# Performance work log

Measured on AMD Instinct MI355X. Metric: run time of the kernel, lower is better.

## Reference

```python
import jax, jax.numpy as jnp
import numpy as np

B, S, H, NH, HD, F, L = 512, 32, 1024, 16, 64, 2048, 6
OBS_D, REF_D, ACT_D, MAX_REL = 256, 128, 32, 32
SCALE = 1.0 / np.sqrt(HD)
LN_EPS = 1e-5


def _ln(x, g, b):
    mu = x.mean(-1, keepdims=True)
    var = ((x - mu) ** 2).mean(-1, keepdims=True)
    return (x - mu) * jax.lax.rsqrt(var + LN_EPS) * g + b


def _mlp3(x, w0, b0, w1, b1, w2, b2):
    h = jax.nn.relu(x @ w0 + b0)
    h = jax.nn.relu(h @ w1 + b1)
    return h @ w2 + b2


def setup_inputs() -> dict:
    key = jax.random.key(0)
    ks = iter(jax.random.split(key, 64))

    def n(shape, scale=1.0):
        return (jax.random.normal(next(ks), shape, dtype=jnp.float32) * scale)

    W = 0.02  # weight scale (xavier-ish) to keep activations sane
    inp = {
        'obs': n((B, S, OBS_D)), 'ref': n((B, S, REF_D)),
        'obs_w0': n((OBS_D, 512), W), 'obs_b0': jnp.zeros((512,), jnp.float32),
        'obs_w1': n((512, 256), W), 'obs_b1': jnp.zeros((256,), jnp.float32),
        'obs_w2': n((256, H), W), 'obs_b2': jnp.zeros((H,), jnp.float32),
        'ref_w0': n((REF_D, 256), W), 'ref_b0': jnp.zeros((256,), jnp.float32),
        'ref_w1': n((256, 256), W), 'ref_b1': jnp.zeros((256,), jnp.float32),
        'ref_w2': n((256, H), W), 'ref_b2': jnp.zeros((H,), jnp.float32),
        'pos_emb': n((64, H), W),
        'Wq': n((L, H, H), W), 'Wk': n((L, H, H), W), 'Wv': n((L, H, H), W),
        'Wo': n((L, H, H), W), 'bo': jnp.zeros((L, H), jnp.float32),
        'rel_emb': n((L, 2 * MAX_REL + 1, HD), W),
        'ff_w1': n((L, H, F), W), 'ff_b1': jnp.zeros((L, F), jnp.float32),
        'ff_w2': n((L, F, H), W), 'ff_b2': jnp.zeros((L, H), jnp.float32),
        'ln1_g': jnp.ones((L, H), jnp.float32), 'ln1_b': jnp.zeros((L, H), jnp.float32),
        'ln2_g': jnp.ones((L, H), jnp.float32), 'ln2_b': jnp.zeros((L, H), jnp.float32),
        'act_w0': n((H, 256), W), 'act_b0': jnp.zeros((256,), jnp.float32),
        'act_w1': n((256, 128), W), 'act_b1': jnp.zeros((128,), jnp.float32),
        'act_w2': n((128, ACT_D), W), 'act_b2': jnp.zeros((ACT_D,), jnp.float32),
    }
    return inp


def _forward(obs, ref, obs_w0, obs_b0, obs_w1, obs_b1, obs_w2, obs_b2,
             ref_w0, ref_b0, ref_w1, ref_b1, ref_w2, ref_b2, pos_emb,
             Wq, Wk, Wv, Wo, bo, rel_emb, ff_w1, ff_b1, ff_w2, ff_b2,
             ln1_g, ln1_b, ln2_g, ln2_b,
             act_w0, act_b0, act_w1, act_b1, act_w2, act_b2):
    b, s, _ = obs.shape
    x = _mlp3(obs, obs_w0, obs_b0, obs_w1, obs_b1, obs_w2, obs_b2)
    x = x + _mlp3(ref, ref_w0, ref_b0, ref_w1, ref_b1, ref_w2, ref_b2)
    x = x + pos_emb[:s][None]  # learned positional encoding

    idx = jnp.arange(s)
    rel_idx = jnp.clip(idx[:, None] - idx[None, :], -MAX_REL, MAX_REL) + MAX_REL  # [S,S]

    def block(h, p):
        wq, wk, wv, wo, b_o, rel, w1, b1, w2, b2, g1, be1, g2, be2 = p
        xn = _ln(h, g1, be1)
        q = (xn @ wq).reshape(b, s, NH, HD)
        k = (xn @ wk).reshape(b, s, NH, HD)
        v = (xn @ wv).reshape(b, s, NH, HD)
        scores = jnp.einsum('bqhd,bkhd->bhqk', q, k) * SCALE
        rel_e = rel[rel_idx]  # [S,S,HD]
        scores = scores + jnp.einsum('bqhd,qkd->bhqk', q, rel_e)
        attn = jax.nn.softmax(scores, axis=-1)
        o = jnp.einsum('bhqk,bkhd->bqhd', attn, v).reshape(b, s, H)
        h = h + o @ wo + b_o
        xn2 = _ln(h, g2, be2)
        ff = jax.nn.gelu(xn2 @ w1 + b1, approximate=False) @ w2 + b2
        return h + ff, None

    x, _ = jax.lax.scan(block, x, (Wq, Wk, Wv, Wo, bo, rel_emb,
                                    ff_w1, ff_b1, ff_w2, ff_b2,
                                    ln1_g, ln1_b, ln2_g, ln2_b))
    return _mlp3(x[:, -1], act_w0, act_b0, act_w1, act_b1, act_w2, act_b2)


def reference(obs, ref, obs_w0, obs_b0, obs_w1, obs_b1, obs_w2, obs_b2,
              ref_w0, ref_b0, ref_w1, ref_b1, ref_w2, ref_b2, pos_emb,
              Wq, Wk, Wv, Wo, bo, rel_emb, ff_w1, ff_b1, ff_w2, ff_b2,
              ln1_g, ln1_b, ln2_g, ln2_b,
              act_w0, act_b0, act_w1, act_b1, act_w2, act_b2):
    return _forward(obs, ref, obs_w0, obs_b0, obs_w1, obs_b1, obs_w2, obs_b2,
                    ref_w0, ref_b0, ref_w1, ref_b1, ref_w2, ref_b2, pos_emb,
                    Wq, Wk, Wv, Wo, bo, rel_emb, ff_w1, ff_b1, ff_w2, ff_b2,
                    ln1_g, ln1_b, ln2_g, ln2_b,
                    act_w0, act_b0, act_w1, act_b1, act_w2, act_b2)
```

## Files before the change

### kernel.cpp

```cpp
#include <hip/hip_runtime.h>
#include <cstdint>
#include <cstddef>

typedef unsigned short u16;
typedef float f32x4 __attribute__((ext_vector_type(4)));
typedef short s16x8 __attribute__((ext_vector_type(8)));
typedef __bf16 bf16x8 __attribute__((ext_vector_type(8)));

#define DEVINL __device__ __forceinline__

DEVINL float bf2f(u16 u){ union{unsigned int i; float f;} c; c.i=((unsigned int)u)<<16; return c.f; }
DEVINL u16 f2bf(float f){ union{float f; unsigned int i;} c; c.f=f; unsigned int u=c.i;
                          u += 0x7FFF + ((u>>16)&1); return (u16)(u>>16); }

DEVINL f32x4 mfma16(bf16x8 a, bf16x8 b, f32x4 c){
  return __builtin_amdgcn_mfma_f32_16x16x32_bf16(a, b, c, 0, 0, 0);
}

typedef const __attribute__((address_space(1))) void* gas1p;
typedef __attribute__((address_space(3))) void* as3p;
DEVINL void async16(const void* g, void* l){
  __builtin_amdgcn_global_load_lds((gas1p)g, (as3p)l, 16, 0, 0);
}


__global__ void cvt_bf16(const float* __restrict__ in, u16* __restrict__ out, int n){
  int i = (blockIdx.x * 256 + threadIdx.x) * 4;
  if (i >= n) return;
  float4 v = *(const float4*)(in + i);
  short4 sv = make_short4((short)f2bf(v.x), (short)f2bf(v.y), (short)f2bf(v.z), (short)f2bf(v.w));
  *(short4*)(out + i) = sv;
}

__global__ __launch_bounds__(256) void trans_w(const float* __restrict__ W, u16* __restrict__ WT,
                                               int K, int N){
  __shared__ float t[32][33];
  const float* Wm = W  + (size_t)blockIdx.z * K * N;
  u16*         Tm = WT + (size_t)blockIdx.z * K * N;
  const int x = threadIdx.x, y = threadIdx.y;
  const int n0 = blockIdx.x * 32, k0 = blockIdx.y * 32;
#pragma unroll
  for (int j = 0; j < 32; j += 8)
    t[y + j][x] = Wm[(size_t)(k0 + y + j) * N + n0 + x];
  __syncthreads();
#pragma unroll
  for (int j = 0; j < 32; j += 8)
    Tm[(size_t)(n0 + y + j) * K + k0 + x] = f2bf(t[x][y + j]);
}


__global__ __launch_bounds__(256) void gemm128(
    const u16* __restrict__ A, const u16* __restrict__ BT,
    const float* __restrict__ bias, const float* __restrict__ resid,
    const float* __restrict__ pos, void* __restrict__ out,
    int M, int N, int K, int fuse)
{
  __shared__ u16 As[2][4096];
  __shared__ u16 Bs[2][4096];
  const int tid = threadIdx.x;

  const int nbn = gridDim.x;
  const int nwg = gridDim.x * gridDim.y;
  const int lid = blockIdx.y * nbn + blockIdx.x;
  const int q8 = nwg >> 3, r8 = nwg & 7;
  const int xcd = lid & 7, posi = lid >> 3;
  const int swz = (xcd < r8 ? xcd * (q8 + 1) : r8 * (q8 + 1) + (xcd - r8) * q8) + posi;
  const int bm = swz / nbn, bn = swz - bm * nbn;

  const int lane = tid & 63, wid = tid >> 6;
  const int lr = lane & 15, lk = lane >> 4;
  const int wm = (wid >> 1) * 64, wn = (wid & 1) * 64;

  f32x4 acc[4][4] = {};

  const int r0 = tid >> 2;
  const int c0 = (tid & 3) * 8;
  const u16* Ab = A  + (size_t)(bm * 128 + r0) * K + c0;
  const u16* Bb = BT + (size_t)(bn * 128 + r0) * K + c0;
  const size_t rstep = (size_t)64 * K;
  const int nk = K >> 5;

  async16(Ab,         &As[0][tid * 8]);
  async16(Ab + rstep, &As[0][2048 + tid * 8]);
  async16(Bb,         &Bs[0][tid * 8]);
  async16(Bb + rstep, &Bs[0][2048 + tid * 8]);

  int cur = 0;
  for (int kt = 0; kt < nk; ++kt){
    __syncthreads();
    if (kt + 1 < nk){
      const u16* An = Ab + (size_t)(kt + 1) * 32;
      const u16* Bn = Bb + (size_t)(kt + 1) * 32;
      u16* Asn = &As[cur ^ 1][0];
      u16* Bsn = &Bs[cur ^ 1][0];
      async16(An,         Asn + tid * 8);
      async16(An + rstep, Asn + 2048 + tid * 8);
      async16(Bn,         Bsn + tid * 8);
      async16(Bn + rstep, Bsn + 2048 + tid * 8);
    }
    bf16x8 af[4], bfv[4];
#pragma unroll
    for (int i = 0; i < 4; ++i)
      af[i] = *(const bf16x8*)&As[cur][(wm + i * 16 + lr) * 32 + lk * 8];
#pragma unroll
    for (int j = 0; j < 4; ++j)
      bfv[j] = *(const bf16x8*)&Bs[cur][(wn + j * 16 + lr) * 32 + lk * 8];
#pragma unroll
    for (int i = 0; i < 4; ++i)
#pragma unroll
      for (int j = 0; j < 4; ++j)
        acc[i][j] = mfma16(af[i], bfv[j], acc[i][j]);
    cur ^= 1;
  }

  const int gm0 = bm * 128 + wm, gn0 = bn * 128 + wn;
  float* outf = (float*)out;
  u16*   outb = (u16*)out;
#pragma unroll
  for (int i = 0; i < 4; ++i){
#pragma unroll
    for (int j = 0; j < 4; ++j){
      const int col = gn0 + j * 16 + lr;
      const float bv = bias ? bias[col] : 0.f;
#pragma unroll
      for (int r = 0; r < 4; ++r){
        const int row = gm0 + i * 16 + lk * 4 + r;
        const size_t idx = (size_t)row * N + col;
        float v = acc[i][j][r] + bv;
        if (fuse == 1)      v = fmaxf(v, 0.f);
        else if (fuse == 2) v = 0.5f * v * (1.f + erff(v * 0.70710678118654752f));
        else if (fuse == 4) v += resid[idx];
        else if (fuse == 5) v += resid[idx] + pos[((row & 31) << 10) + col];
        if (fuse >= 3) outf[idx] = v;
        else           outb[idx] = f2bf(v);
      }
    }
  }
}


__global__ __launch_bounds__(256) void ln_k(
    const float* __restrict__ x, const float* __restrict__ g,
    const float* __restrict__ b, u16* __restrict__ out)
{
  const int row = blockIdx.x;
  const float* xr = x + (size_t)row * 1024;
  const int tid = threadIdx.x;
  float4 v = *(const float4*)(xr + tid * 4);
  float s  = v.x + v.y + v.z + v.w;
  float ss = v.x * v.x + v.y * v.y + v.z * v.z + v.w * v.w;
#pragma unroll
  for (int m = 1; m < 64; m <<= 1){ s += __shfl_xor(s, m, 64); ss += __shfl_xor(ss, m, 64); }
  __shared__ float red[8];
  if ((tid & 63) == 0){ red[tid >> 6] = s; red[4 + (tid >> 6)] = ss; }
  __syncthreads();
  s  = red[0] + red[1] + red[2] + red[3];
  ss = red[4] + red[5] + red[6] + red[7];
  const float mu = s * (1.f / 1024.f);
  const float rs = rsqrtf(ss * (1.f / 1024.f) - mu * mu + 1e-5f);
  float4 gg = *(const float4*)(g + tid * 4);
  float4 bb = *(const float4*)(b + tid * 4);
  short4 sv = make_short4((short)f2bf((v.x - mu) * rs * gg.x + bb.x),
                          (short)f2bf((v.y - mu) * rs * gg.y + bb.y),
                          (short)f2bf((v.z - mu) * rs * gg.z + bb.z),
                          (short)f2bf((v.w - mu) * rs * gg.w + bb.w));
  *(short4*)(out + (size_t)row * 1024 + tid * 4) = sv;
}


__global__ __launch_bounds__(256) void attn_k(
    const u16* __restrict__ QKV, const u16* __restrict__ rel,
    u16* __restrict__ O)
{
  __shared__ char smem[65536];
  const int tid = threadIdx.x;
  const int wid = tid >> 6, lane = tid & 63;
  const int lr = lane & 15, lk = lane >> 4;
  char* sw = smem + wid * 16384;
  float* P = (float*)sw;
  u16*  AL = (u16*)(sw + 8704);
  u16*  VT = (u16*)(sw + 11264);

  const int pair = blockIdx.x * 4 + wid;
  const int b = pair >> 4, h = pair & 15;
  const u16* q  = QKV + (size_t)b * 32 * 3072 + (size_t)h * 64;
  const u16* kk = q + 1024;
  const u16* v  = q + 2048;
  u16* o = O + (size_t)b * 32768 + (size_t)h * 64;

  s16x8 vv[4];
#pragma unroll
  for (int j = 0; j < 4; ++j){
    const int e = j * 64 + lane;
    const int ki = e >> 3, d0 = (e & 7) * 8;
    vv[j] = *(const s16x8*)(v + (size_t)ki * 3072 + d0);
  }

  bf16x8 qf[2][2], kf[2][2];
#pragma unroll
  for (int mf = 0; mf < 2; ++mf)
#pragma unroll
    for (int ks = 0; ks < 2; ++ks){
      qf[mf][ks] = *(const bf16x8*)(q  + (size_t)(mf * 16 + lr) * 3072 + ks * 32 + lk * 8);
      kf[mf][ks] = *(const bf16x8*)(kk + (size_t)(mf * 16 + lr) * 3072 + ks * 32 + lk * 8);
    }

  f32x4 sc[2][2] = {};
#pragma unroll
  for (int mf = 0; mf < 2; ++mf)
#pragma unroll
    for (int nf = 0; nf < 2; ++nf){
      sc[mf][nf] = mfma16(qf[mf][0], kf[nf][0], sc[mf][nf]);
      sc[mf][nf] = mfma16(qf[mf][1], kf[nf][1], sc[mf][nf]);
      sc[mf][nf] *= 0.125f;
    }

  f32x4 p[2][4] = {};
#pragma unroll
  for (int nf = 0; nf < 4; ++nf){
    bf16x8 rf0 = *(const bf16x8*)(rel + (nf * 16 + lr) * 64 + lk * 8);
    bf16x8 rf1 = *(const bf16x8*)(rel + (nf * 16 + lr) * 64 + 32 + lk * 8);
#pragma unroll
    for (int mf = 0; mf < 2; ++mf){
      p[mf][nf] = mfma16(qf[mf][0], rf0, p[mf][nf]);
      p[mf][nf] = mfma16(qf[mf][1], rf1, p[mf][nf]);
    }
  }

#pragma unroll
  for (int j = 0; j < 4; ++j){
    const int e = j * 64 + lane;
    const int ki = e >> 3, d0 = (e & 7) * 8;
#pragma unroll
    for (int i = 0; i < 8; ++i)
      VT[(d0 + i) * 40 + ki] = (u16)vv[j][i];
  }
#pragma unroll
  for (int mf = 0; mf < 2; ++mf)
#pragma unroll
    for (int nf = 0; nf < 4; ++nf)
#pragma unroll
      for (int r = 0; r < 4; ++r)
        P[(mf * 16 + lk * 4 + r) * 68 + nf * 16 + lr] = p[mf][nf][r];

  __syncthreads();

#pragma unroll
  for (int mf = 0; mf < 2; ++mf)
#pragma unroll
    for (int n2 = 0; n2 < 2; ++n2)
#pragma unroll
      for (int r = 0; r < 4; ++r){
        const int qr = mf * 16 + lk * 4 + r;
        const int kc = n2 * 16 + lr;
        sc[mf][n2][r] += P[qr * 68 + (qr - kc + 32)];
      }

#pragma unroll
  for (int mf = 0; mf < 2; ++mf)
#pragma unroll
    for (int r = 0; r < 4; ++r){
      float mx = fmaxf(sc[mf][0][r], sc[mf][1][r]);
#pragma unroll
      for (int m2 = 1; m2 < 16; m2 <<= 1) mx = fmaxf(mx, __shfl_xor(mx, m2, 64));
      const float e0 = __expf(sc[mf][0][r] - mx);
      const float e1 = __expf(sc[mf][1][r] - mx);
      float sm = e0 + e1;
#pragma unroll
      for (int m2 = 1; m2 < 16; m2 <<= 1) sm += __shfl_xor(sm, m2, 64);
      const float inv = 1.f / sm;
      sc[mf][0][r] = e0 * inv;
      sc[mf][1][r] = e1 * inv;
    }

#pragma unroll
  for (int mf = 0; mf < 2; ++mf)
#pragma unroll
    for (int n2 = 0; n2 < 2; ++n2)
#pragma unroll
      for (int r = 0; r < 4; ++r)
        AL[(mf * 16 + lk * 4 + r) * 40 + n2 * 16 + lr] = f2bf(sc[mf][n2][r]);

  __syncthreads();

  bf16x8 paf[2];
  paf[0] = *(const bf16x8*)&AL[(lr) * 40 + lk * 8];
  paf[1] = *(const bf16x8*)&AL[(16 + lr) * 40 + lk * 8];

  f32x4 of[2][4] = {};
#pragma unroll
  for (int nf = 0; nf < 4; ++nf){
    bf16x8 vf = *(const bf16x8*)&VT[(nf * 16 + lr) * 40 + lk * 8];
    of[0][nf] = mfma16(paf[0], vf, of[0][nf]);
    of[1][nf] = mfma16(paf[1], vf, of[1][nf]);
  }
#pragma unroll
  for (int mf = 0; mf < 2; ++mf)
#pragma unroll
    for (int nf = 0; nf < 4; ++nf)
#pragma unroll
      for (int r = 0; r < 4; ++r)
        o[(size_t)(mf * 16 + lk * 4 + r) * 1024 + nf * 16 + lr] = f2bf(of[mf][nf][r]);
}


__global__ void gather_last(const float* __restrict__ x, u16* __restrict__ out){
  const int i = blockIdx.x * 256 + threadIdx.x;
  const int b = i >> 10, c = i & 1023;
  out[i] = f2bf(x[((size_t)b * 32 + 31) * 1024 + c]);
}

__global__ void small_gemm(const u16* __restrict__ A, const u16* __restrict__ BT,
                           const float* __restrict__ bias, void* __restrict__ out,
                           int M, int N, int K, int fuse){
  const int idx = blockIdx.x * 256 + threadIdx.x;
  if (idx >= M * N) return;
  const int m = idx / N, n = idx - m * N;
  const u16* a  = A  + (size_t)m * K;
  const u16* bt = BT + (size_t)n * K;
  float acc = 0.f;
  for (int k = 0; k < K; k += 8){
    s16x8 av = *(const s16x8*)(a + k);
    s16x8 bv = *(const s16x8*)(bt + k);
#pragma unroll
    for (int i = 0; i < 8; ++i) acc += bf2f((u16)av[i]) * bf2f((u16)bv[i]);
  }
  float v = acc + bias[n];
  if (fuse == 1) v = fmaxf(v, 0.f);
  if (fuse == 3) ((float*)out)[idx] = v;
  else           ((u16*)out)[idx]   = f2bf(v);
}


extern "C" void kernel_launch(void* const* d_in, const int* in_sizes, int n_in,
                              void* d_out, int out_size, void* d_ws, size_t ws_size,
                              hipStream_t stream)
{
  (void)in_sizes; (void)n_in; (void)out_size;
  const float* obs    = (const float*)d_in[0];
  const float* refp   = (const float*)d_in[1];
  const float* obs_w0 = (const float*)d_in[2];
  const float* obs_b0 = (const float*)d_in[3];
  const float* obs_w1 = (const float*)d_in[4];
  const float* obs_b1 = (const float*)d_in[5];
  const float* obs_w2 = (const float*)d_in[6];
  const float* obs_b2 = (const float*)d_in[7];
  const float* ref_w0 = (const float*)d_in[8];
  const float* ref_b0 = (const float*)d_in[9];
  const float* ref_w1 = (const float*)d_in[10];
  const float* ref_b1 = (const float*)d_in[11];
  const float* ref_w2 = (const float*)d_in[12];
  const float* ref_b2 = (const float*)d_in[13];
  const float* pos    = (const float*)d_in[14];
  const float* Wq     = (const float*)d_in[15];
  const float* Wk     = (const float*)d_in[16];
  const float* Wv     = (const float*)d_in[17];
  const float* Wo     = (const float*)d_in[18];
  const float* bo     = (const float*)d_in[19];
  const float* rel    = (const float*)d_in[20];
  const float* ff_w1  = (const float*)d_in[21];
  const float* ff_b1  = (const float*)d_in[22];
  const float* ff_w2  = (const float*)d_in[23];
  const float* ff_b2  = (const float*)d_in[24];
  const float* ln1g   = (const float*)d_in[25];
  const float* ln1b   = (const float*)d_in[26];
  const float* ln2g   = (const float*)d_in[27];
  const float* ln2b   = (const float*)d_in[28];
  const float* act_w0 = (const float*)d_in[29];
  const float* act_b0 = (const float*)d_in[30];
  const float* act_w1 = (const float*)d_in[31];
  const float* act_b1 = (const float*)d_in[32];
  const float* act_w2 = (const float*)d_in[33];
  const float* act_b2 = (const float*)d_in[34];
  float* outp = (float*)d_out;

  char* wsp = (char*)d_ws; size_t off = 0;
  auto alloc = [&](size_t bytes)->char*{ char* p = wsp + off;
                                         off = (off + bytes + 255) & ~(size_t)255; return p; };

  u16* wt_obs0 = (u16*)alloc((size_t)512 * 256 * 2);
  u16* wt_obs1 = (u16*)alloc((size_t)256 * 512 * 2);
  u16* wt_obs2 = (u16*)alloc((size_t)1024 * 256 * 2);
  u16* wt_ref0 = (u16*)alloc((size_t)256 * 128 * 2);
  u16* wt_ref1 = (u16*)alloc((size_t)256 * 256 * 2);
  u16* wt_ref2 = (u16*)alloc((size_t)1024 * 256 * 2);
  u16* wt_a0   = (u16*)alloc((size_t)256 * 1024 * 2);
  u16* wt_a1   = (u16*)alloc((size_t)128 * 256 * 2);
  u16* wt_a2   = (u16*)alloc((size_t)32 * 128 * 2);
  u16* rel_bf  = (u16*)alloc((size_t)6 * 65 * 64 * 2);
  u16* wt_qkv  = (u16*)alloc((size_t)3072 * 1024 * 2);
  u16* wt_lo   = (u16*)alloc((size_t)1024 * 1024 * 2);
  u16* wt_lf1  = (u16*)alloc((size_t)2048 * 1024 * 2);
  u16* wt_lf2  = (u16*)alloc((size_t)2048 * 1024 * 2);
  float* x     = (float*)alloc((size_t)16384 * 1024 * 4);
  u16* xn      = (u16*)alloc((size_t)16384 * 1024 * 2);
  u16* qkv     = (u16*)alloc((size_t)16384 * 3072 * 2);

  if (off > ws_size) return;

  u16* obs_bf = qkv;
  u16* h1     = qkv + (size_t)16384 * 256;
  u16* h2     = qkv + (size_t)16384 * 768;
  u16* ref_bf = xn;
  u16* ob     = xn;
  u16* ffb    = qkv;
  u16* xlast  = qkv;
  u16* a1b    = qkv + (size_t)16384 * 256;
  u16* a2b    = qkv + (size_t)16384 * 512;

  auto CV = [&](const float* src, u16* dst, int n){
    cvt_bf16<<<dim3((n / 4 + 255) / 256), dim3(256), 0, stream>>>(src, dst, n);
  };
  auto TR = [&](const float* W, u16* WT, int Kd, int Nd, int nz){
    trans_w<<<dim3(Nd / 32, Kd / 32, nz), dim3(32, 8), 0, stream>>>(W, WT, Kd, Nd);
  };
  auto GM = [&](const u16* A, const u16* BT, const float* bias, const float* resid,
                const float* posb, void* op, int Md, int Nd, int Kd, int fuse){
    gemm128<<<dim3(Nd / 128, Md / 128), dim3(256), 0, stream>>>(A, BT, bias, resid, posb, op, Md, Nd, Kd, fuse);
  };

  CV(rel, rel_bf, 6 * 65 * 64);
  TR(obs_w0, wt_obs0, 256, 512, 1);
  TR(obs_w1, wt_obs1, 512, 256, 1);
  TR(obs_w2, wt_obs2, 256, 1024, 1);
  TR(ref_w0, wt_ref0, 128, 256, 1);
  TR(ref_w1, wt_ref1, 256, 256, 1);
  TR(ref_w2, wt_ref2, 256, 1024, 1);
  TR(act_w0, wt_a0, 1024, 256, 1);
  TR(act_w1, wt_a1, 256, 128, 1);
  TR(act_w2, wt_a2, 128, 32, 1);

  const int M = 16384;
  CV(obs, obs_bf, 16384 * 256);
  GM(obs_bf, wt_obs0, obs_b0, nullptr, nullptr, h1, M, 512, 256, 1);
  GM(h1,     wt_obs1, obs_b1, nullptr, nullptr, h2, M, 256, 512, 1);
  GM(h2,     wt_obs2, obs_b2, nullptr, nullptr, x,  M, 1024, 256, 3);
  CV(refp, ref_bf, 16384 * 128);
  GM(ref_bf, wt_ref0, ref_b0, nullptr, nullptr, h2, M, 256, 128, 1);
  GM(h2,     wt_ref1, ref_b1, nullptr, nullptr, h1, M, 256, 256, 1);
  GM(h1,     wt_ref2, ref_b2, x, pos,           x,  M, 1024, 256, 5);

  for (int l = 0; l < 6; ++l){
    TR(Wq + (size_t)l * 1048576, wt_qkv,                        1024, 1024, 1);
    TR(Wk + (size_t)l * 1048576, wt_qkv + (size_t)1024 * 1024,  1024, 1024, 1);
    TR(Wv + (size_t)l * 1048576, wt_qkv + (size_t)2048 * 1024,  1024, 1024, 1);
    TR(Wo + (size_t)l * 1048576, wt_lo, 1024, 1024, 1);
    TR(ff_w1 + (size_t)l * 2097152, wt_lf1, 1024, 2048, 1);
    TR(ff_w2 + (size_t)l * 2097152, wt_lf2, 2048, 1024, 1);

    ln_k<<<dim3(16384), dim3(256), 0, stream>>>(x, ln1g + l * 1024, ln1b + l * 1024, xn);
    GM(xn, wt_qkv, nullptr, nullptr, nullptr, qkv, M, 3072, 1024, 0);
    attn_k<<<dim3(2048), dim3(256), 0, stream>>>(qkv, rel_bf + (size_t)l * 4160, ob);
    GM(ob, wt_lo, bo + l * 1024, x, nullptr, x, M, 1024, 1024, 4);
    ln_k<<<dim3(16384), dim3(256), 0, stream>>>(x, ln2g + l * 1024, ln2b + l * 1024, xn);
    GM(xn,  wt_lf1, ff_b1 + l * 2048, nullptr, nullptr, ffb, M, 2048, 1024, 2);
    GM(ffb, wt_lf2, ff_b2 + l * 1024, x, nullptr, x, M, 1024, 2048, 4);
  }

  gather_last<<<dim3(2048), dim3(256), 0, stream>>>(x, xlast);
  small_gemm<<<dim3(512 * 256 / 256), dim3(256), 0, stream>>>(xlast, wt_a0, act_b0, a1b, 512, 256, 1024, 1);
  small_gemm<<<dim3(512 * 128 / 256), dim3(256), 0, stream>>>(a1b, wt_a1, act_b1, a2b, 512, 128, 256, 1);
  small_gemm<<<dim3(512 * 32 / 256),  dim3(256), 0, stream>>>(a2b, wt_a2, act_b2, outp, 512, 32, 128, 3);
}
```

Measured before the change: 3.981 ms.

## Add 256x256-tile 8-wave GEMM with swizzled LDS and XCD-aware block remap

Adds a gemm256 kernel with 512 threads and 256x256 output tiles. It uses a double-buffered LDS staged via global_load_lds with an XOR swizzle, a four-phase MFMA schedule interleaved with prefetch, setprio hints, and a workgroup remap that groups tiles per XCD. It replaces gemm128 for all large-N GEMMs (QKV, Wo, FFN, and the obs/ref final layers). The larger tiles are meant to raise arithmetic intensity and cut global/L2 traffic, at the cost of higher register and LDS pressure, fewer workgroups per GEMM, and many barriers.

```diff
diff --git a/kernel.cpp b/kernel.cpp
--- a/kernel.cpp
+++ b/kernel.cpp
@@ -22,6 +22,8 @@
 DEVINL void async16(const void* g, void* l){
   __builtin_amdgcn_global_load_lds((gas1p)g, (as3p)l, 16, 0, 0);
 }
+
+#define SWZ(b) ((b) ^ ((((b) >> 9) & 1) << 5))
 
 
 __global__ void cvt_bf16(const float* __restrict__ in, u16* __restrict__ out, int n){
@@ -127,6 +129,173 @@
         const int row = gm0 + i * 16 + lk * 4 + r;
         const size_t idx = (size_t)row * N + col;
         float v = acc[i][j][r] + bv;
+        if (fuse == 1)      v = fmaxf(v, 0.f);
+        else if (fuse == 2) v = 0.5f * v * (1.f + erff(v * 0.70710678118654752f));
+        else if (fuse == 4) v += resid[idx];
+        else if (fuse == 5) v += resid[idx] + pos[((row & 31) << 10) + col];
+        if (fuse >= 3) outf[idx] = v;
+        else           outb[idx] = f2bf(v);
+      }
+    }
+  }
+}
+
+
+#define QUAD256(mh, nh)                                                        \
+  { _Pragma("unroll") for (int mi = 0; mi < 4; ++mi)                           \
+    _Pragma("unroll") for (int nj = 0; nj < 2; ++nj)                           \
+      _Pragma("unroll") for (int s = 0; s < 2; ++s)                            \
+        acc[(mh)*4+mi][(nh)*2+nj] =                                            \
+          mfma16(af[mi][s], bq[(nh)*2+nj][s], acc[(mh)*4+mi][(nh)*2+nj]); }
+
+__global__ __launch_bounds__(512, 2) void gemm256(
+    const u16* __restrict__ A, const u16* __restrict__ BT,
+    const float* __restrict__ bias, const float* __restrict__ resid,
+    const float* __restrict__ pos, void* __restrict__ out,
+    int M, int N, int K, int fuse)
+{
+  __shared__ u16 Al[2][2][8192];
+  __shared__ u16 Bl[2][2][8192];
+  const int tid = threadIdx.x;
+
+  const int nbn = gridDim.x, nwg = gridDim.x * gridDim.y;
+  const int lid = blockIdx.y * nbn + blockIdx.x;
+  const int q8 = nwg >> 3, r8 = nwg & 7;
+  const int xcd = lid & 7, posi = lid >> 3;
+  const int swz = (xcd < r8 ? xcd * (q8 + 1) : r8 * (q8 + 1) + (xcd - r8) * q8) + posi;
+  const int bm = swz / nbn, bn = swz - bm * nbn;
+
+  const int lane = tid & 63, wid = tid >> 6;
+  const int wm = wid >> 2, wn = wid & 3;
+  const int lr = lane & 15, lk = lane >> 4;
+  const int brow = (wn & 1) * 64;
+
+  f32x4 acc[8][4] = {};
+  bf16x8 af[4][2], bq[4][2];
+
+  const int nt = K >> 6;
+
+  auto stageA = [&](int buf, int kt){
+#pragma unroll
+    for (int h = 0; h < 2; ++h){
+      const char* g = (const char*)(A + (size_t)(bm * 256 + h * 128) * K + kt * 64);
+      char* l = (char*)&Al[buf][h][0];
+#pragma unroll
+      for (int j = 0; j < 2; ++j){
+        const int L = (j * 512 + tid) * 16;
+        const int lg = SWZ(L);
+        async16(g + (size_t)(lg >> 7) * ((size_t)K * 2) + (lg & 127), l + L);
+      }
+    }
+  };
+  auto stageB = [&](int buf, int kt){
+#pragma unroll
+    for (int h = 0; h < 2; ++h){
+      const char* g = (const char*)(BT + (size_t)(bn * 256 + h * 128) * K + kt * 64);
+      char* l = (char*)&Bl[buf][h][0];
+#pragma unroll
+      for (int j = 0; j < 2; ++j){
+        const int L = (j * 512 + tid) * 16;
+        const int lg = SWZ(L);
+        async16(g + (size_t)(lg >> 7) * ((size_t)K * 2) + (lg & 127), l + L);
+      }
+    }
+  };
+
+  stageA(0, 0); stageB(0, 0);
+  stageA(1, 1); stageB(1, 1);
+  asm volatile("s_waitcnt vmcnt(8)" ::: "memory");
+  __builtin_amdgcn_s_barrier();
+
+  for (int t = 0; t < nt; ++t){
+    const int p = t & 1;
+    const char* Ab = (const char*)&Al[p][wm][0];
+    const char* Bb = (const char*)&Bl[p][wn >> 1][0];
+
+#pragma unroll
+    for (int mi = 0; mi < 4; ++mi)
+#pragma unroll
+      for (int s = 0; s < 2; ++s){
+        const int lg = (mi * 16 + lr) * 128 + s * 64 + lk * 16;
+        af[mi][s] = *(const bf16x8*)(Ab + SWZ(lg));
+      }
+#pragma unroll
+    for (int nj = 0; nj < 2; ++nj)
+#pragma unroll
+      for (int s = 0; s < 2; ++s){
+        const int lg = (brow + nj * 16 + lr) * 128 + s * 64 + lk * 16;
+        bq[nj][s] = *(const bf16x8*)(Bb + SWZ(lg));
+      }
+    __builtin_amdgcn_s_barrier();
+    asm volatile("s_waitcnt lgkmcnt(0)" ::: "memory");
+    __builtin_amdgcn_sched_barrier(0);
+    __builtin_amdgcn_s_setprio(1);
+    QUAD256(0, 0);
+    __builtin_amdgcn_s_setprio(0);
+    __builtin_amdgcn_sched_barrier(0);
+    __builtin_amdgcn_s_barrier();
+
+#pragma unroll
+    for (int nj = 0; nj < 2; ++nj)
+#pragma unroll
+      for (int s = 0; s < 2; ++s){
+        const int lg = (brow + 32 + nj * 16 + lr) * 128 + s * 64 + lk * 16;
+        bq[2 + nj][s] = *(const bf16x8*)(Bb + SWZ(lg));
+      }
+    __builtin_amdgcn_s_barrier();
+    asm volatile("s_waitcnt lgkmcnt(0)" ::: "memory");
+    __builtin_amdgcn_sched_barrier(0);
+    __builtin_amdgcn_s_setprio(1);
+    QUAD256(0, 1);
+    __builtin_amdgcn_s_setprio(0);
+    __builtin_amdgcn_sched_barrier(0);
+    __builtin_amdgcn_s_barrier();
+
+#pragma unroll
+    for (int mi = 0; mi < 4; ++mi)
+#pragma unroll
+      for (int s = 0; s < 2; ++s){
+        const int lg = (64 + mi * 16 + lr) * 128 + s * 64 + lk * 16;
+        af[mi][s] = *(const bf16x8*)(Ab + SWZ(lg));
+      }
+    if (t + 2 < nt) stageB(p, t + 2);
+    __builtin_amdgcn_s_barrier();
+    asm volatile("s_waitcnt lgkmcnt(0)" ::: "memory");
+    __builtin_amdgcn_sched_barrier(0);
+    __builtin_amdgcn_s_setprio(1);
+    QUAD256(1, 0);
+    __builtin_amdgcn_s_setprio(0);
+    __builtin_amdgcn_sched_barrier(0);
+    __builtin_amdgcn_s_barrier();
+
+    if (t + 2 < nt) stageA(p, t + 2);
+    __builtin_amdgcn_s_barrier();
+    __builtin_amdgcn_s_setprio(1);
+    QUAD256(1, 1);
+    __builtin_amdgcn_s_setprio(0);
+    __builtin_amdgcn_sched_barrier(0);
+    if (t + 2 < nt)      asm volatile("s_waitcnt vmcnt(8)" ::: "memory");
+    else if (t + 1 < nt) asm volatile("s_waitcnt vmcnt(0)" ::: "memory");
+    __builtin_amdgcn_sched_barrier(0);
+    __builtin_amdgcn_s_barrier();
+  }
+
+  const int gm0 = bm * 256 + wm * 128, gn0 = bn * 256 + wn * 64;
+  float* outf = (float*)out;
+  u16*   outb = (u16*)out;
+  float bv[4];
+#pragma unroll
+  for (int j = 0; j < 4; ++j) bv[j] = bias ? bias[gn0 + j * 16 + lr] : 0.f;
+#pragma unroll
+  for (int m = 0; m < 8; ++m){
+#pragma unroll
+    for (int j = 0; j < 4; ++j){
+      const int col = gn0 + j * 16 + lr;
+#pragma unroll
+      for (int r = 0; r < 4; ++r){
+        const int row = gm0 + m * 16 + lk * 4 + r;
+        const size_t idx = (size_t)row * N + col;
+        float v = acc[m][j][r] + bv[j];
         if (fuse == 1)      v = fmaxf(v, 0.f);
         else if (fuse == 2) v = 0.5f * v * (1.f + erff(v * 0.70710678118654752f));
         else if (fuse == 4) v += resid[idx];
@@ -418,6 +587,10 @@
                 const float* posb, void* op, int Md, int Nd, int Kd, int fuse){
     gemm128<<<dim3(Nd / 128, Md / 128), dim3(256), 0, stream>>>(A, BT, bias, resid, posb, op, Md, Nd, Kd, fuse);
   };
+  auto GM2 = [&](const u16* A, const u16* BT, const float* bias, const float* resid,
+                 const float* posb, void* op, int Md, int Nd, int Kd, int fuse){
+    gemm256<<<dim3(Nd / 256, Md / 256), dim3(512), 0, stream>>>(A, BT, bias, resid, posb, op, Md, Nd, Kd, fuse);
+  };
 
   CV(rel, rel_bf, 6 * 65 * 64);
   TR(obs_w0, wt_obs0, 256, 512, 1);
@@ -434,11 +607,11 @@
   CV(obs, obs_bf, 16384 * 256);
   GM(obs_bf, wt_obs0, obs_b0, nullptr, nullptr, h1, M, 512, 256, 1);
   GM(h1,     wt_obs1, obs_b1, nullptr, nullptr, h2, M, 256, 512, 1);
-  GM(h2,     wt_obs2, obs_b2, nullptr, nullptr, x,  M, 1024, 256, 3);
+  GM2(h2,    wt_obs2, obs_b2, nullptr, nullptr, x,  M, 1024, 256, 3);
   CV(refp, ref_bf, 16384 * 128);
   GM(ref_bf, wt_ref0, ref_b0, nullptr, nullptr, h2, M, 256, 128, 1);
   GM(h2,     wt_ref1, ref_b1, nullptr, nullptr, h1, M, 256, 256, 1);
-  GM(h1,     wt_ref2, ref_b2, x, pos,           x,  M, 1024, 256, 5);
+  GM2(h1,    wt_ref2, ref_b2, x, pos,           x,  M, 1024, 256, 5);
 
   for (int l = 0; l < 6; ++l){
     TR(Wq + (size_t)l * 1048576, wt_qkv,                        1024, 1024, 1);
@@ -449,12 +622,12 @@
     TR(ff_w2 + (size_t)l * 2097152, wt_lf2, 2048, 1024, 1);
 
     ln_k<<<dim3(16384), dim3(256), 0, stream>>>(x, ln1g + l * 1024, ln1b + l * 1024, xn);
-    GM(xn, wt_qkv, nullptr, nullptr, nullptr, qkv, M, 3072, 1024, 0);
+    GM2(xn, wt_qkv, nullptr, nullptr, nullptr, qkv, M, 3072, 1024, 0);
     attn_k<<<dim3(2048), dim3(256), 0, stream>>>(qkv, rel_bf + (size_t)l * 4160, ob);
-    GM(ob, wt_lo, bo + l * 1024, x, nullptr, x, M, 1024, 1024, 4);
+    GM2(ob, wt_lo, bo + l * 1024, x, nullptr, x, M, 1024, 1024, 4);
     ln_k<<<dim3(16384), dim3(256), 0, stream>>>(x, ln2g + l * 1024, ln2b + l * 1024, xn);
-    GM(xn,  wt_lf1, ff_b1 + l * 2048, nullptr, nullptr, ffb, M, 2048, 1024, 2);
-    GM(ffb, wt_lf2, ff_b2 + l * 1024, x, nullptr, x, M, 1024, 2048, 4);
+    GM2(xn,  wt_lf1, ff_b1 + l * 2048, nullptr, nullptr, ffb, M, 2048, 1024, 2);
+    GM2(ffb, wt_lf2, ff_b2 + l * 1024, x, nullptr, x, M, 1024, 2048, 4);
   }
 
   gather_last<<<dim3(2048), dim3(256), 0, stream>>>(x, xlast);
```

New measurement: 3.784 ms. 4.9% less time.
